# Kernel tuning notes

Hardware: AMD Instinct MI355X
Metric: run time of the kernel (lower is better)

Reference implementation:

```python
import jax, jax.numpy as jnp
import numpy as np

TOPOLOGY = [-1, 0, 0, 0, 1, 2, 3, 4, 5, 6, 7, 8, 9, 9, 9, 12, 13, 14, 16, 17, 18, 19, 20, 21]
JOINT_WEIGHTS = np.ones(24, dtype=np.float32)
B1 = 1.0
B2 = 1.0


def quaternion_to_matrix(q):
    # pytorch3d convention: real part first (w, x, y, z)
    w, x, y, z = q[..., 0], q[..., 1], q[..., 2], q[..., 3]
    two_s = 2.0 / jnp.sum(q * q, axis=-1)
    o = jnp.stack([
        1 - two_s * (y * y + z * z), two_s * (x * y - z * w), two_s * (x * z + y * w),
        two_s * (x * y + z * w), 1 - two_s * (x * x + z * z), two_s * (y * z - x * w),
        two_s * (x * z - y * w), two_s * (y * z + x * w), 1 - two_s * (x * x + y * y),
    ], axis=-1)
    return o.reshape(q.shape[:-1] + (3, 3))


def fk(topology, X_m, X_t):
    # X_m: (bs, T, J*4+3), X_t: (bs, J, 3)
    J = len(topology)
    quat = X_m[..., :-3].reshape(X_m.shape[:-1] + (J, 4))
    local_rot = quaternion_to_matrix(quat)          # (bs, T, J, 3, 3)
    grots = [None] * J
    gtrs = [None] * J
    grots[0] = local_rot[..., 0, :, :]
    gtrs[0] = X_m[..., -3:]                          # root translation
    for i in range(1, J):
        pi = topology[i]
        grots[i] = jnp.matmul(grots[pi], local_rot[..., i, :, :])
        gtrs[i] = jnp.einsum('btij,bj->bti', grots[pi], X_t[:, i]) + gtrs[pi]
    return jnp.stack(grots, axis=-3), jnp.stack(gtrs, axis=-2)


def split_raw_motion(raw_motion):
    position = raw_motion[..., -3:]
    rotation = raw_motion[..., :-3]
    rotation = rotation.reshape(rotation.shape[:-1] + (-1, 4))
    norm = jnp.linalg.norm(rotation, axis=-1, keepdims=True)
    rotation = rotation / jnp.maximum(norm, 1e-12)
    return rotation, position


def weighted_mse(w, a, b):
    # w: (J,), a/b: (bs, T, J, C) -> per-joint weighted mean squared error
    return jnp.mean(w[None, None, :, None] * (a - b) ** 2)


def setup_inputs() -> dict:
    key = jax.random.key(0)
    k1, k2, k3, k4 = jax.random.split(key, 4)
    bs, T, J = 64, 2048, 24
    return {
        'Y_m': jax.random.normal(k1, (bs, T, J * 4 + 3), dtype=jnp.float32),
        'X_m': jax.random.normal(k2, (bs, T, J * 4 + 3), dtype=jnp.float32),
        'Y_t': jax.random.normal(k3, (bs, J, 3), dtype=jnp.float32),
        'X_t': jax.random.normal(k4, (bs, J, 3), dtype=jnp.float32),
    }


def reference(Y_m, X_m, Y_t, X_t):
    w = jnp.asarray(JOINT_WEIGHTS)
    rot_x, pos_x = split_raw_motion(X_m)
    rot_y, pos_y = split_raw_motion(Y_m)
    grot_y, gtr_y = fk(TOPOLOGY, Y_m, Y_t)
    grot_x, gtr_x = fk(TOPOLOGY, X_m, X_t)
    loss_rot = B1 * weighted_mse(w, rot_y, rot_x)
    loss_fk = B2 * (2.5 * weighted_mse(w, gtr_y, gtr_x)
                    + jnp.mean((pos_y - pos_x) ** 2))
    return loss_rot + loss_fk
```

## Files before the change

### kernel.cpp

```cpp
#include <hip/hip_runtime.h>

#define BS 64
#define TT 2048
#define NJ 24
#define ROWF 99
#define TROWS 128
#define BLOCK 128
#define NROWS (BS * TT)

__device__ __forceinline__ void quat2mat(float w, float x, float y, float z, float* R) {
  float s = 2.0f / (w*w + x*x + y*y + z*z);
  float xx = s*x*x, yy = s*y*y, zz = s*z*z;
  float xy = s*x*y, xz = s*x*z, yz = s*y*z;
  float xw = s*x*w, yw = s*y*w, zw = s*z*w;
  R[0] = 1.0f - (yy+zz); R[1] = xy - zw;        R[2] = xz + yw;
  R[3] = xy + zw;        R[4] = 1.0f - (xx+zz); R[5] = yz - xw;
  R[6] = xz - yw;        R[7] = yz + xw;        R[8] = 1.0f - (xx+yy);
}

__device__ __forceinline__ void mm3(const float* A, const float* B, float* C) {
#pragma unroll
  for (int r = 0; r < 3; ++r) {
#pragma unroll
    for (int c = 0; c < 3; ++c) {
      C[3*r+c] = fmaf(A[3*r], B[c], fmaf(A[3*r+1], B[3+c], A[3*r+2]*B[6+c]));
    }
  }
}

template<int PHASE>
__device__ __forceinline__ void fk_chain(const float* __restrict__ rowp,
                                         const float* __restrict__ tvec,
                                         float* __restrict__ gtr, float& gacc) {
  float G0[9], Ga[9], Gb[9], G9[9];
  float T0[3], Ta[3], Tb[3], T9[3];

  quat2mat(rowp[0], rowp[1], rowp[2], rowp[3], G0);
  T0[0] = rowp[96]; T0[1] = rowp[97]; T0[2] = rowp[98];
  if (PHASE == 0) { gtr[0] = T0[0]; gtr[1] = T0[1]; gtr[2] = T0[2]; }
  else { float d0 = T0[0]-gtr[0], d1 = T0[1]-gtr[1], d2 = T0[2]-gtr[2];
         gacc += d0*d0 + d1*d1 + d2*d2; }

#define STEP(c, Gp, Tp, Go, To) do { \
    float R[9]; quat2mat(rowp[4*(c)], rowp[4*(c)+1], rowp[4*(c)+2], rowp[4*(c)+3], R); \
    mm3(Gp, R, Go); \
    To[0] = fmaf(Gp[0], tvec[3*(c)], fmaf(Gp[1], tvec[3*(c)+1], fmaf(Gp[2], tvec[3*(c)+2], Tp[0]))); \
    To[1] = fmaf(Gp[3], tvec[3*(c)], fmaf(Gp[4], tvec[3*(c)+1], fmaf(Gp[5], tvec[3*(c)+2], Tp[1]))); \
    To[2] = fmaf(Gp[6], tvec[3*(c)], fmaf(Gp[7], tvec[3*(c)+1], fmaf(Gp[8], tvec[3*(c)+2], Tp[2]))); \
    if (PHASE == 0) { gtr[3*(c)] = To[0]; gtr[3*(c)+1] = To[1]; gtr[3*(c)+2] = To[2]; } \
    else { float d0 = To[0]-gtr[3*(c)], d1 = To[1]-gtr[3*(c)+1], d2 = To[2]-gtr[3*(c)+2]; \
           gacc += d0*d0 + d1*d1 + d2*d2; } \
  } while (0)

  STEP(1,  G0, T0, Ga, Ta); STEP(4,  Ga, Ta, Gb, Tb); STEP(7,  Gb, Tb, Ga, Ta); STEP(10, Ga, Ta, Gb, Tb);
  STEP(2,  G0, T0, Ga, Ta); STEP(5,  Ga, Ta, Gb, Tb); STEP(8,  Gb, Tb, Ga, Ta); STEP(11, Ga, Ta, Gb, Tb);
  STEP(3,  G0, T0, Ga, Ta); STEP(6,  Ga, Ta, Gb, Tb); STEP(9,  Gb, Tb, G9, T9);
  STEP(12, G9, T9, Ga, Ta); STEP(15, Ga, Ta, Gb, Tb);
  STEP(13, G9, T9, Ga, Ta); STEP(16, Ga, Ta, Gb, Tb); STEP(18, Gb, Tb, Ga, Ta); STEP(20, Ga, Ta, Gb, Tb); STEP(22, Gb, Tb, Ga, Ta);
  STEP(14, G9, T9, Ga, Ta); STEP(17, Ga, Ta, Gb, Tb); STEP(19, Gb, Tb, Ga, Ta); STEP(21, Ga, Ta, Gb, Tb); STEP(23, Gb, Tb, Ga, Ta);
#undef STEP
}

__global__ __launch_bounds__(BLOCK, 2) void motion_loss_kernel(
    const float* __restrict__ Ym, const float* __restrict__ Xm,
    const float* __restrict__ Yt, const float* __restrict__ Xt,
    float* __restrict__ out) {
  __shared__ __align__(16) float tile[TROWS * ROWF];
  __shared__ float tX[NJ * 3], tY[NJ * 3];

  const int tid = threadIdx.x;
  const int blk = blockIdx.x;
  const size_t row0 = (size_t)blk * TROWS;
  const int b = blk / (TT / TROWS);

  if (tid < NJ * 3) {
    tX[tid] = Xt[(size_t)b * NJ * 3 + tid];
    tY[tid] = Yt[(size_t)b * NJ * 3 + tid];
  }

  {
    const float4* g4 = (const float4*)(Xm + row0 * ROWF);
    float4* l4 = (float4*)tile;
    for (int k = tid; k < TROWS * ROWF / 4; k += BLOCK) l4[k] = g4[k];
  }
  __syncthreads();

  float gtrX[NJ * 3];
  float gacc = 0.0f, dummy = 0.0f;
  const float* rowp = tile + tid * ROWF;
  fk_chain<0>(rowp, tX, gtrX, dummy);
  __syncthreads();

  float rot_acc = 0.0f, pos_acc = 0.0f;
  const float* __restrict__ Yg = Ym + row0 * ROWF;
#pragma unroll 4
  for (int k = 0; k < NJ; ++k) {
    int q = tid + k * BLOCK;
    int r = q / NJ;
    int j = q - r * NJ;
    int off = r * ROWF + 4 * j;
    float y0 = Yg[off], y1 = Yg[off+1], y2 = Yg[off+2], y3 = Yg[off+3];
    float x0 = tile[off], x1 = tile[off+1], x2 = tile[off+2], x3 = tile[off+3];
    float ny = fmaxf(sqrtf(y0*y0 + y1*y1 + y2*y2 + y3*y3), 1e-12f);
    float nx = fmaxf(sqrtf(x0*x0 + x1*x1 + x2*x2 + x3*x3), 1e-12f);
    float iy = 1.0f / ny, ix = 1.0f / nx;
    float d0 = y0*iy - x0*ix, d1 = y1*iy - x1*ix;
    float d2 = y2*iy - x2*ix, d3 = y3*iy - x3*ix;
    rot_acc += d0*d0 + d1*d1 + d2*d2 + d3*d3;
    tile[off] = y0; tile[off+1] = y1; tile[off+2] = y2; tile[off+3] = y3;
  }
#pragma unroll
  for (int k = 0; k < 3; ++k) {
    int e = tid + k * BLOCK;
    int r = e / 3;
    int c = e - r * 3;
    int off = r * ROWF + 96 + c;
    float y = Yg[off], x = tile[off];
    float d = y - x;
    pos_acc += d * d;
    tile[off] = y;
  }
  __syncthreads();

  fk_chain<1>(rowp, tY, gtrX, gacc);

  const float c_rot = 1.0f / ((float)NROWS * NJ * 4);
  const float c_gtr = 2.5f / ((float)NROWS * NJ * 3);
  const float c_pos = 1.0f / ((float)NROWS * 3);
  float contrib = c_rot * rot_acc + c_gtr * gacc + c_pos * pos_acc;
#pragma unroll
  for (int o = 32; o > 0; o >>= 1) contrib += __shfl_down(contrib, o, 64);
  if ((tid & 63) == 0) atomicAdd(out, contrib);
}

extern "C" void kernel_launch(void* const* d_in, const int* in_sizes, int n_in,
                              void* d_out, int out_size, void* d_ws, size_t ws_size,
                              hipStream_t stream) {
  const float* Ym = (const float*)d_in[0];
  const float* Xm = (const float*)d_in[1];
  const float* Yt = (const float*)d_in[2];
  const float* Xt = (const float*)d_in[3];
  float* out = (float*)d_out;
  hipMemsetAsync(out, 0, sizeof(float), stream);
  motion_loss_kernel<<<NROWS / TROWS, BLOCK, 0, stream>>>(Ym, Xm, Yt, Xt, out);
}
```

Measured before the change: 170.7 us.

## Fuse X and Y forward kinematics into one register pass without shared tiles

Drops the shared-memory tile staging and the two separate FK passes. Each thread now reads its own X and Y rows straight from global memory with float4 loads and walks both kinematic chains together. It keeps only three parent-slot transforms in registers and accumulates the translation difference directly, so per-joint global translations are no longer stored. This removes the 50KB of LDS per block, the barriers and the 72-float gtr array, which should raise occupancy. The trade-off is strided, uncoalesced and possibly unaligned float4 loads per thread, which lean on cache reuse.

```diff
diff --git a/kernel.cpp b/kernel.cpp
--- a/kernel.cpp
+++ b/kernel.cpp
@@ -4,15 +4,19 @@
 #define TT 2048
 #define NJ 24
 #define ROWF 99
-#define TROWS 128
 #define BLOCK 128
 #define NROWS (BS * TT)
 
-__device__ __forceinline__ void quat2mat(float w, float x, float y, float z, float* R) {
-  float s = 2.0f / (w*w + x*x + y*y + z*z);
-  float xx = s*x*x, yy = s*y*y, zz = s*z*z;
-  float xy = s*x*y, xz = s*x*z, yz = s*y*z;
-  float xw = s*x*w, yw = s*y*w, zw = s*z*w;
+__device__ __forceinline__ void ld4u(const float* __restrict__ p, float* q) {
+  const float4 v = *reinterpret_cast<const float4*>(p);
+  q[0] = v.x; q[1] = v.y; q[2] = v.z; q[3] = v.w;
+}
+
+__device__ __forceinline__ void quat2mat_s(const float* q, float s, float* R) {
+  const float w = q[0], x = q[1], y = q[2], z = q[3];
+  const float xx = s*x*x, yy = s*y*y, zz = s*z*z;
+  const float xy = s*x*y, xz = s*x*z, yz = s*y*z;
+  const float xw = s*x*w, yw = s*y*w, zw = s*z*w;
   R[0] = 1.0f - (yy+zz); R[1] = xy - zw;        R[2] = xz + yw;
   R[3] = xy + zw;        R[4] = 1.0f - (xx+zz); R[5] = yz - xw;
   R[6] = xz - yw;        R[7] = yz + xw;        R[8] = 1.0f - (xx+yy);
@@ -28,106 +32,102 @@
   }
 }
 
-template<int PHASE>
-__device__ __forceinline__ void fk_chain(const float* __restrict__ rowp,
-                                         const float* __restrict__ tvec,
-                                         float* __restrict__ gtr, float& gacc) {
-  float G0[9], Ga[9], Gb[9], G9[9];
-  float T0[3], Ta[3], Tb[3], T9[3];
-
-  quat2mat(rowp[0], rowp[1], rowp[2], rowp[3], G0);
-  T0[0] = rowp[96]; T0[1] = rowp[97]; T0[2] = rowp[98];
-  if (PHASE == 0) { gtr[0] = T0[0]; gtr[1] = T0[1]; gtr[2] = T0[2]; }
-  else { float d0 = T0[0]-gtr[0], d1 = T0[1]-gtr[1], d2 = T0[2]-gtr[2];
-         gacc += d0*d0 + d1*d1 + d2*d2; }
-
-#define STEP(c, Gp, Tp, Go, To) do { \
-    float R[9]; quat2mat(rowp[4*(c)], rowp[4*(c)+1], rowp[4*(c)+2], rowp[4*(c)+3], R); \
-    mm3(Gp, R, Go); \
-    To[0] = fmaf(Gp[0], tvec[3*(c)], fmaf(Gp[1], tvec[3*(c)+1], fmaf(Gp[2], tvec[3*(c)+2], Tp[0]))); \
-    To[1] = fmaf(Gp[3], tvec[3*(c)], fmaf(Gp[4], tvec[3*(c)+1], fmaf(Gp[5], tvec[3*(c)+2], Tp[1]))); \
-    To[2] = fmaf(Gp[6], tvec[3*(c)], fmaf(Gp[7], tvec[3*(c)+1], fmaf(Gp[8], tvec[3*(c)+2], Tp[2]))); \
-    if (PHASE == 0) { gtr[3*(c)] = To[0]; gtr[3*(c)+1] = To[1]; gtr[3*(c)+2] = To[2]; } \
-    else { float d0 = To[0]-gtr[3*(c)], d1 = To[1]-gtr[3*(c)+1], d2 = To[2]-gtr[3*(c)+2]; \
-           gacc += d0*d0 + d1*d1 + d2*d2; } \
-  } while (0)
-
-  STEP(1,  G0, T0, Ga, Ta); STEP(4,  Ga, Ta, Gb, Tb); STEP(7,  Gb, Tb, Ga, Ta); STEP(10, Ga, Ta, Gb, Tb);
-  STEP(2,  G0, T0, Ga, Ta); STEP(5,  Ga, Ta, Gb, Tb); STEP(8,  Gb, Tb, Ga, Ta); STEP(11, Ga, Ta, Gb, Tb);
-  STEP(3,  G0, T0, Ga, Ta); STEP(6,  Ga, Ta, Gb, Tb); STEP(9,  Gb, Tb, G9, T9);
-  STEP(12, G9, T9, Ga, Ta); STEP(15, Ga, Ta, Gb, Tb);
-  STEP(13, G9, T9, Ga, Ta); STEP(16, Ga, Ta, Gb, Tb); STEP(18, Gb, Tb, Ga, Ta); STEP(20, Ga, Ta, Gb, Tb); STEP(22, Gb, Tb, Ga, Ta);
-  STEP(14, G9, T9, Ga, Ta); STEP(17, Ga, Ta, Gb, Tb); STEP(19, Gb, Tb, Ga, Ta); STEP(21, Ga, Ta, Gb, Tb); STEP(23, Gb, Tb, Ga, Ta);
-#undef STEP
-}
-
 __global__ __launch_bounds__(BLOCK, 2) void motion_loss_kernel(
     const float* __restrict__ Ym, const float* __restrict__ Xm,
     const float* __restrict__ Yt, const float* __restrict__ Xt,
     float* __restrict__ out) {
-  __shared__ __align__(16) float tile[TROWS * ROWF];
-  __shared__ float tX[NJ * 3], tY[NJ * 3];
+  const int tid = threadIdx.x;
+  const size_t row = (size_t)blockIdx.x * BLOCK + tid;
+  const int b = (int)(row / TT);
+  const float* __restrict__ xr = Xm + row * ROWF;
+  const float* __restrict__ yr = Ym + row * ROWF;
+  const float* __restrict__ tX = Xt + (size_t)b * NJ * 3;
+  const float* __restrict__ tY = Yt + (size_t)b * NJ * 3;
 
-  const int tid = threadIdx.x;
-  const int blk = blockIdx.x;
-  const size_t row0 = (size_t)blk * TROWS;
-  const int b = blk / (TT / TROWS);
+  float GX[3][9], GY[3][9], D[3][3];
+  float rot_acc = 0.0f, gtr_acc = 0.0f, pos_acc = 0.0f;
 
-  if (tid < NJ * 3) {
-    tX[tid] = Xt[(size_t)b * NJ * 3 + tid];
-    tY[tid] = Yt[(size_t)b * NJ * 3 + tid];
+  {
+    float xq[4], yq[4];
+    ld4u(xr, xq); ld4u(yr, yq);
+    const float qqx = xq[0]*xq[0] + xq[1]*xq[1] + xq[2]*xq[2] + xq[3]*xq[3];
+    const float qqy = yq[0]*yq[0] + yq[1]*yq[1] + yq[2]*yq[2] + yq[3]*yq[3];
+    const float ix = 1.0f / fmaxf(sqrtf(qqx), 1e-12f);
+    const float iy = 1.0f / fmaxf(sqrtf(qqy), 1e-12f);
+    const float r0 = yq[0]*iy - xq[0]*ix, r1 = yq[1]*iy - xq[1]*ix;
+    const float r2 = yq[2]*iy - xq[2]*ix, r3 = yq[3]*iy - xq[3]*ix;
+    rot_acc += r0*r0 + r1*r1 + r2*r2 + r3*r3;
+    quat2mat_s(xq, 2.0f / qqx, GX[0]);
+    quat2mat_s(yq, 2.0f / qqy, GY[0]);
+    float xp[4], yp[4];
+    ld4u(xr + 95, xp); ld4u(yr + 95, yp);
+    D[0][0] = yp[1] - xp[1]; D[0][1] = yp[2] - xp[2]; D[0][2] = yp[3] - xp[3];
+    const float d2 = D[0][0]*D[0][0] + D[0][1]*D[0][1] + D[0][2]*D[0][2];
+    gtr_acc += d2;
+    pos_acc = d2;
   }
 
-  {
-    const float4* g4 = (const float4*)(Xm + row0 * ROWF);
-    float4* l4 = (float4*)tile;
-    for (int k = tid; k < TROWS * ROWF / 4; k += BLOCK) l4[k] = g4[k];
-  }
-  __syncthreads();
+#define JSTEP(j, PS, NS) do {                                                  \
+    float xq[4], yq[4];                                                        \
+    ld4u(xr + 4*(j), xq); ld4u(yr + 4*(j), yq);                                \
+    const float qqx = xq[0]*xq[0] + xq[1]*xq[1] + xq[2]*xq[2] + xq[3]*xq[3];   \
+    const float qqy = yq[0]*yq[0] + yq[1]*yq[1] + yq[2]*yq[2] + yq[3]*yq[3];   \
+    const float ix = 1.0f / fmaxf(sqrtf(qqx), 1e-12f);                         \
+    const float iy = 1.0f / fmaxf(sqrtf(qqy), 1e-12f);                         \
+    const float r0 = yq[0]*iy - xq[0]*ix, r1 = yq[1]*iy - xq[1]*ix;            \
+    const float r2 = yq[2]*iy - xq[2]*ix, r3 = yq[3]*iy - xq[3]*ix;            \
+    rot_acc += r0*r0 + r1*r1 + r2*r2 + r3*r3;                                  \
+    const float tx0 = tX[3*(j)], tx1 = tX[3*(j)+1], tx2 = tX[3*(j)+2];         \
+    const float ty0 = tY[3*(j)], ty1 = tY[3*(j)+1], ty2 = tY[3*(j)+2];         \
+    const float vx0 = fmaf(GX[PS][0],tx0, fmaf(GX[PS][1],tx1, GX[PS][2]*tx2)); \
+    const float vx1 = fmaf(GX[PS][3],tx0, fmaf(GX[PS][4],tx1, GX[PS][5]*tx2)); \
+    const float vx2 = fmaf(GX[PS][6],tx0, fmaf(GX[PS][7],tx1, GX[PS][8]*tx2)); \
+    const float vy0 = fmaf(GY[PS][0],ty0, fmaf(GY[PS][1],ty1, GY[PS][2]*ty2)); \
+    const float vy1 = fmaf(GY[PS][3],ty0, fmaf(GY[PS][4],ty1, GY[PS][5]*ty2)); \
+    const float vy2 = fmaf(GY[PS][6],ty0, fmaf(GY[PS][7],ty1, GY[PS][8]*ty2)); \
+    const float d0 = D[PS][0] + (vy0 - vx0);                                   \
+    const float d1 = D[PS][1] + (vy1 - vx1);                                   \
+    const float d2 = D[PS][2] + (vy2 - vx2);                                   \
+    gtr_acc += d0*d0 + d1*d1 + d2*d2;                                          \
+    float RX[9], RY[9], GnX[9], GnY[9];                                        \
+    quat2mat_s(xq, 2.0f / qqx, RX);                                            \
+    quat2mat_s(yq, 2.0f / qqy, RY);                                            \
+    mm3(GX[PS], RX, GnX);                                                      \
+    mm3(GY[PS], RY, GnY);                                                      \
+    _Pragma("unroll")                                                          \
+    for (int k = 0; k < 9; ++k) { GX[NS][k] = GnX[k]; GY[NS][k] = GnY[k]; }    \
+    D[NS][0] = d0; D[NS][1] = d1; D[NS][2] = d2;                               \
+  } while (0)
 
-  float gtrX[NJ * 3];
-  float gacc = 0.0f, dummy = 0.0f;
-  const float* rowp = tile + tid * ROWF;
-  fk_chain<0>(rowp, tX, gtrX, dummy);
-  __syncthreads();
-
-  float rot_acc = 0.0f, pos_acc = 0.0f;
-  const float* __restrict__ Yg = Ym + row0 * ROWF;
-#pragma unroll 4
-  for (int k = 0; k < NJ; ++k) {
-    int q = tid + k * BLOCK;
-    int r = q / NJ;
-    int j = q - r * NJ;
-    int off = r * ROWF + 4 * j;
-    float y0 = Yg[off], y1 = Yg[off+1], y2 = Yg[off+2], y3 = Yg[off+3];
-    float x0 = tile[off], x1 = tile[off+1], x2 = tile[off+2], x3 = tile[off+3];
-    float ny = fmaxf(sqrtf(y0*y0 + y1*y1 + y2*y2 + y3*y3), 1e-12f);
-    float nx = fmaxf(sqrtf(x0*x0 + x1*x1 + x2*x2 + x3*x3), 1e-12f);
-    float iy = 1.0f / ny, ix = 1.0f / nx;
-    float d0 = y0*iy - x0*ix, d1 = y1*iy - x1*ix;
-    float d2 = y2*iy - x2*ix, d3 = y3*iy - x3*ix;
-    rot_acc += d0*d0 + d1*d1 + d2*d2 + d3*d3;
-    tile[off] = y0; tile[off+1] = y1; tile[off+2] = y2; tile[off+3] = y3;
-  }
-#pragma unroll
-  for (int k = 0; k < 3; ++k) {
-    int e = tid + k * BLOCK;
-    int r = e / 3;
-    int c = e - r * 3;
-    int off = r * ROWF + 96 + c;
-    float y = Yg[off], x = tile[off];
-    float d = y - x;
-    pos_acc += d * d;
-    tile[off] = y;
-  }
-  __syncthreads();
-
-  fk_chain<1>(rowp, tY, gtrX, gacc);
+  JSTEP( 1, 0, 1);
+  JSTEP( 2, 0, 2);
+  JSTEP( 3, 0, 0);
+  JSTEP( 4, 1, 1);
+  JSTEP( 5, 2, 2);
+  JSTEP( 6, 0, 0);
+  JSTEP( 7, 1, 1);
+  JSTEP( 8, 2, 2);
+  JSTEP( 9, 0, 0);
+  JSTEP(10, 1, 1);
+  JSTEP(11, 2, 2);
+  JSTEP(12, 0, 1);
+  JSTEP(13, 0, 2);
+  JSTEP(14, 0, 0);
+  JSTEP(15, 1, 1);
+  JSTEP(16, 2, 2);
+  JSTEP(17, 0, 0);
+  JSTEP(18, 2, 2);
+  JSTEP(19, 0, 0);
+  JSTEP(20, 2, 2);
+  JSTEP(21, 0, 0);
+  JSTEP(22, 2, 2);
+  JSTEP(23, 0, 0);
+#undef JSTEP
 
   const float c_rot = 1.0f / ((float)NROWS * NJ * 4);
   const float c_gtr = 2.5f / ((float)NROWS * NJ * 3);
   const float c_pos = 1.0f / ((float)NROWS * 3);
-  float contrib = c_rot * rot_acc + c_gtr * gacc + c_pos * pos_acc;
+  float contrib = c_rot * rot_acc + c_gtr * gtr_acc + c_pos * pos_acc;
 #pragma unroll
   for (int o = 32; o > 0; o >>= 1) contrib += __shfl_down(contrib, o, 64);
   if ((tid & 63) == 0) atomicAdd(out, contrib);
@@ -142,5 +142,5 @@
   const float* Xt = (const float*)d_in[3];
   float* out = (float*)d_out;
   hipMemsetAsync(out, 0, sizeof(float), stream);
-  motion_loss_kernel<<<NROWS / TROWS, BLOCK, 0, stream>>>(Ym, Xm, Yt, Xt, out);
+  motion_loss_kernel<<<NROWS / BLOCK, BLOCK, 0, stream>>>(Ym, Xm, Yt, Xt, out);
 }
```

Result: no change. 169.5 us (-0.7%).
